# Optimization experiments

Measured on AMD Instinct MI355X. Metric: run time of the kernel, lower is better.

The kernel has to match this reference:

```python
import jax, jax.numpy as jnp
import numpy as np

D = 1024
H = 16
HD = D // H
MLP = 4 * D


def _lin(key, fin, fout):
    k1, k2 = jax.random.split(key)
    lim = 1.0 / np.sqrt(fin)
    W = jax.random.uniform(k1, (fin, fout), minval=-lim, maxval=lim, dtype=jnp.float32)
    b = jax.random.uniform(k2, (fout,), minval=-lim, maxval=lim, dtype=jnp.float32)
    return W, b


def setup_inputs() -> dict:
    key = jax.random.key(0)
    ks = jax.random.split(key, 10)
    x = jax.random.normal(ks[0], (4, 2048, D), dtype=jnp.float32)
    time_emb = jax.random.normal(ks[1], (4, D), dtype=jnp.float32)
    Wqkv, bqkv = _lin(ks[2], D, 3 * D)
    Wproj, bproj = _lin(ks[3], D, D)
    W1, b1 = _lin(ks[4], D, MLP)
    W2, b2 = _lin(ks[5], MLP, D)
    Wt, bt = _lin(ks[6], D, 6 * D)
    g1 = jnp.ones((D,), jnp.float32); be1 = jnp.zeros((D,), jnp.float32)
    g2 = jnp.ones((D,), jnp.float32); be2 = jnp.zeros((D,), jnp.float32)
    return {"x": x, "time_emb": time_emb, "Wqkv": Wqkv, "bqkv": bqkv,
            "Wproj": Wproj, "bproj": bproj, "W1": W1, "b1": b1, "W2": W2, "b2": b2,
            "Wt": Wt, "bt": bt, "g1": g1, "be1": be1, "g2": g2, "be2": be2}


def layernorm(x, g, b, eps=1e-5):
    mu = jnp.mean(x, axis=-1, keepdims=True)
    var = jnp.var(x, axis=-1, keepdims=True)
    return (x - mu) * jax.lax.rsqrt(var + eps) * g + b


def attention(h, Wqkv, bqkv, Wproj, bproj):
    B, L, _ = h.shape
    qkv = (h @ Wqkv + bqkv).reshape(B, L, 3, H, HD)
    q, k, v = jnp.moveaxis(qkv, 2, 0)  # each [B,L,H,HD]
    scale = HD ** -0.5
    attn = jnp.einsum('blhd,bmhd->bhlm', q, k) * scale
    attn = jax.nn.softmax(attn, axis=-1)
    out = jnp.einsum('bhlm,bmhd->blhd', attn, v).reshape(B, L, D)
    return out @ Wproj + bproj


def reference(x, time_emb, Wqkv, bqkv, Wproj, bproj, W1, b1, W2, b2, Wt, bt, g1, be1, g2, be2):
    tp = (jax.nn.silu(time_emb) @ Wt + bt)[:, None, :]  # [B,1,6D]
    shift_msa, scale_msa, gate_msa, shift_mlp, scale_mlp, gate_mlp = jnp.split(tp, 6, axis=-1)
    h = layernorm(x, g1, be1)
    h = h * (1.0 + scale_msa) + shift_msa
    h = attention(h, Wqkv, bqkv, Wproj, bproj)
    x = x + gate_msa * h
    h = layernorm(x, g2, be2)
    h = h * (1.0 + scale_mlp) + shift_mlp
    h = jax.nn.gelu(h @ W1 + b1, approximate=False) @ W2 + b2
    x = x + gate_mlp * h
    return x
```

## Files before the change

kernel.cpp:

```cpp
#include <hip/hip_runtime.h>
#include <hip/hip_bf16.h>
#include <math.h>


typedef __attribute__((ext_vector_type(8))) __bf16 bf16x8;
typedef __attribute__((ext_vector_type(4))) float f32x4;

union FragU { uint4 u; bf16x8 b; };

#define AS1(p) ((const __attribute__((address_space(1))) void*)(p))
#define AS3(p) ((__attribute__((address_space(3))) void*)(p))

__device__ __forceinline__ float bflo(uint u) {
    union { uint i; float f; } v; v.i = u << 16; return v.f;
}
__device__ __forceinline__ ushort f2bf(float f) {
    union { float f; uint i; } v; v.f = f;
    uint r = (v.i + 0x7fffu + ((v.i >> 16) & 1u)) >> 16;
    return (ushort)r;
}
__device__ __forceinline__ uint pkbf(float a, float b) {
    return __builtin_amdgcn_perm(__float_as_uint(b), __float_as_uint(a), 0x07060302u);
}
__device__ __forceinline__ void stval(ushort* p, float v) { *p = f2bf(v); }
__device__ __forceinline__ void stval(float* p, float v) { *p = v; }

__device__ __forceinline__ float gelu_f(float x) {
    float y = 0.7978845608f * (x + 0.044715f * x * x * x);
    float e = exp2f(y * 2.88539008178f);
    float t = 1.f - 2.f / (1.f + e);
    return 0.5f * x * (1.f + t);
}

__global__ __launch_bounds__(256) void transpose_f2b(const float* __restrict__ in,
                                                     ushort* __restrict__ out,
                                                     int R, int C) {
    __shared__ ushort t[32][33];
    int c0 = blockIdx.x * 32, r0 = blockIdx.y * 32;
    int tx = threadIdx.x, ty = threadIdx.y;
#pragma unroll
    for (int i = 0; i < 32; i += 8)
        t[ty + i][tx] = f2bf(in[(size_t)(r0 + ty + i) * C + c0 + tx]);
    __syncthreads();
#pragma unroll
    for (int i = 0; i < 32; i += 8)
        out[(size_t)(c0 + ty + i) * R + r0 + tx] = t[tx][ty + i];
}

__global__ __launch_bounds__(256) void transpose_v(const ushort* __restrict__ qkv,
                                                   ushort* __restrict__ vT) {
    int bh = blockIdx.x >> 5, lt = blockIdx.x & 31;
    int b = bh >> 4, h = bh & 15;
    int d = threadIdx.x & 63, lg = threadIdx.x >> 6;
    const ushort* src = qkv + (size_t)b * 2048 * 3072 + 2048 + h * 64 + d;
#pragma unroll
    for (int g = 0; g < 2; g++) {
        int l0 = lt * 64 + lg * 16 + g * 8;
        ushort v[8];
#pragma unroll
        for (int i = 0; i < 8; i++) v[i] = src[(size_t)(l0 + i) * 3072];
        *(uint4*)&vT[((size_t)bh * 64 + d) * 2048 + l0] = *(uint4*)v;
    }
}

__global__ __launch_bounds__(256) void tp_gemm(const float* __restrict__ te,
                                               const ushort* __restrict__ WtT,
                                               const float* __restrict__ bt,
                                               float* __restrict__ tp) {
    int w = blockIdx.x * 4 + (threadIdx.x >> 6);
    int lane = threadIdx.x & 63;
    int b = w / 6144, n = w % 6144;
    const ushort* wr = WtT + (size_t)n * 1024;
    const float* tr = te + (size_t)b * 1024;
    float s = 0.f;
#pragma unroll
    for (int i = 0; i < 16; i++) {
        int k = lane + 64 * i;
        float t = tr[k];
        float sil = t / (1.f + __expf(-t));
        s += sil * bflo((uint)wr[k]);
    }
#pragma unroll
    for (int x = 32; x; x >>= 1) s += __shfl_xor(s, x);
    if (lane == 0) tp[(size_t)b * 6144 + n] = s + bt[n];
}

__global__ __launch_bounds__(256) void ln_mod(const float* __restrict__ x,
                                              const float* __restrict__ tpb,
                                              const float* __restrict__ g,
                                              const float* __restrict__ be,
                                              ushort* __restrict__ out,
                                              int shift_off, int scale_off) {
    __shared__ float2 sred[4];
    int row = blockIdx.x;
    int b = row >> 11;
    int tid = threadIdx.x;
    float4 f = *(const float4*)&x[(size_t)row * 1024 + tid * 4];
    float v[4] = {f.x, f.y, f.z, f.w};
    float s = v[0] + v[1] + v[2] + v[3];
    float s2 = v[0] * v[0] + v[1] * v[1] + v[2] * v[2] + v[3] * v[3];
#pragma unroll
    for (int m = 32; m; m >>= 1) { s += __shfl_xor(s, m); s2 += __shfl_xor(s2, m); }
    if ((tid & 63) == 0) sred[tid >> 6] = make_float2(s, s2);
    __syncthreads();
    s = sred[0].x + sred[1].x + sred[2].x + sred[3].x;
    s2 = sred[0].y + sred[1].y + sred[2].y + sred[3].y;
    float mu = s * (1.f / 1024.f);
    float var = s2 * (1.f / 1024.f) - mu * mu;
    float rs = rsqrtf(var + 1e-5f);
    const float* tprow = tpb + (size_t)b * 6144;
    ushort o4[4];
#pragma unroll
    for (int t = 0; t < 4; t++) {
        int c = tid * 4 + t;
        float y = (v[t] - mu) * rs * g[c] + be[c];
        y = y * (1.f + tprow[scale_off + c]) + tprow[shift_off + c];
        o4[t] = f2bf(y);
    }
    *(uint2*)&out[(size_t)row * 1024 + tid * 4] = *(uint2*)o4;
}

template <int EPI, typename OT>
__global__ __launch_bounds__(256) void gemm_bt(const ushort* __restrict__ A,
                                               const ushort* __restrict__ BT,
                                               const float* __restrict__ bias,
                                               OT* __restrict__ C,
                                               int M, int N, int K,
                                               const float* __restrict__ res,
                                               const float* __restrict__ tpb,
                                               int goff, int sccols) {
    __shared__ __align__(16) ushort As[2][128 * 32];
    __shared__ __align__(16) ushort Bs[2][128 * 32];
    int m0 = blockIdx.y * 128, n0 = blockIdx.x * 128;
    int tid = threadIdx.x;
    int wid = tid >> 6, lane = tid & 63;
    int wy = wid >> 1, wx = wid & 1;
    int r16 = lane & 15;
    int q8 = (lane >> 4) << 3;

    f32x4 acc[4][4];
#pragma unroll
    for (int i = 0; i < 4; i++)
#pragma unroll
        for (int j = 0; j < 4; j++) acc[i][j] = (f32x4){0.f, 0.f, 0.f, 0.f};

    int sr = tid >> 2;
    int sc = (tid & 3) << 3;
    const ushort* Abase = A + (size_t)(m0 + sr) * K + sc;
    const ushort* Bbase = BT + (size_t)(n0 + sr) * K + sc;

    for (int k0 = 0; k0 < K; k0 += 64) {
#pragma unroll
        for (int c = 0; c < 2; c++) {
            ushort* AsW = As[c] + wid * 512;
            ushort* BsW = Bs[c] + wid * 512;
            int kk = k0 + 32 * c;
            __builtin_amdgcn_global_load_lds(AS1(Abase + kk), AS3(AsW), 16, 0, 0);
            __builtin_amdgcn_global_load_lds(AS1(Abase + (size_t)64 * K + kk), AS3(AsW + 2048), 16, 0, 0);
            __builtin_amdgcn_global_load_lds(AS1(Bbase + kk), AS3(BsW), 16, 0, 0);
            __builtin_amdgcn_global_load_lds(AS1(Bbase + (size_t)64 * K + kk), AS3(BsW + 2048), 16, 0, 0);
        }
        __syncthreads();
#pragma unroll
        for (int c = 0; c < 2; c++) {
            FragU fa[4], fb[4];
#pragma unroll
            for (int i = 0; i < 4; i++)
                fa[i].u = *(const uint4*)&As[c][(wy * 64 + i * 16 + r16) * 32 + q8];
#pragma unroll
            for (int j = 0; j < 4; j++)
                fb[j].u = *(const uint4*)&Bs[c][(wx * 64 + j * 16 + r16) * 32 + q8];
#pragma unroll
            for (int i = 0; i < 4; i++)
#pragma unroll
                for (int j = 0; j < 4; j++)
                    acc[i][j] = __builtin_amdgcn_mfma_f32_16x16x32_bf16(fa[i].b, fb[j].b, acc[i][j], 0, 0, 0);
        }
        __syncthreads();
    }

    int q4 = (lane >> 4) << 2;
#pragma unroll
    for (int i = 0; i < 4; i++) {
#pragma unroll
        for (int j = 0; j < 4; j++) {
            int col = n0 + wx * 64 + j * 16 + r16;
            float bv = bias[col];
#pragma unroll
            for (int t = 0; t < 4; t++) {
                int row = m0 + wy * 64 + i * 16 + q4 + t;
                float v = acc[i][j][t] + bv;
                if constexpr (EPI == 0) {
                    if (col < sccols) v *= 0.18033688011f;
                }
                if constexpr (EPI == 1) {
                    v = gelu_f(v);
                }
                if constexpr (EPI == 2) {
                    float rv = res[(size_t)row * N + col];
                    float gate = tpb[(size_t)(row >> 11) * 6144 + goff + col];
                    v = rv + gate * v;
                }
                stval(&C[(size_t)row * N + col], v);
            }
        }
    }
}

__global__ __launch_bounds__(512, 6) void attn_mfma(const ushort* __restrict__ qkv,
                                                    const ushort* __restrict__ vT,
                                                    ushort* __restrict__ out) {
    __shared__ __align__(16) ushort Ks[2][64 * 72];
    __shared__ __align__(16) ushort Vs[2][64 * 72];
    __shared__ __align__(16) ushort Ps[128 * 72];

    int tid = threadIdx.x;
    int wid = tid >> 6, lane = tid & 63;
    int r16 = lane & 15, quad = lane >> 4;
    int q8 = quad << 3, q4 = quad << 2;

    int bh = blockIdx.x >> 4;
    int qt = blockIdx.x & 15;
    int b = bh >> 4, h = bh & 15;
    const ushort* qkbase = qkv + (size_t)b * 2048 * 3072 + h * 64;

    int kr = tid >> 3;
    int kc = (tid & 7) << 3;
    const ushort* kptr = qkbase + 1024 + (size_t)kr * 3072 + kc;
    const ushort* vptr = vT + (size_t)bh * 131072 + (size_t)kr * 2048 + kc;

    uint4 ka = *(const uint4*)kptr;
    uint4 va = *(const uint4*)vptr;

    {
        int r = tid >> 2;
        int c = (tid & 3) << 4;
        const ushort* qp = qkbase + (size_t)(qt * 128 + r) * 3072 + c;
        *(uint4*)&Ps[r * 72 + c] = *(const uint4*)qp;
        *(uint4*)&Ps[r * 72 + c + 8] = *(const uint4*)(qp + 8);
    }
    __syncthreads();
    FragU qa[2];
#pragma unroll
    for (int ks = 0; ks < 2; ks++)
        qa[ks].u = *(const uint4*)&Ps[(wid * 16 + r16) * 72 + ks * 32 + q8];

    *(uint4*)&Ks[0][kr * 72 + kc] = ka;
    *(uint4*)&Vs[0][kr * 72 + kc] = va;
    ka = *(const uint4*)(kptr + (size_t)64 * 3072);
    va = *(const uint4*)(vptr + 64);
    __syncthreads();

    float l4[4] = {0.f, 0.f, 0.f, 0.f};
    f32x4 o[4];
#pragma unroll
    for (int dn = 0; dn < 4; dn++) o[dn] = (f32x4){0.f, 0.f, 0.f, 0.f};

    for (int kt = 0; kt < 32; kt++) {
        int cur = kt & 1;
        const ushort* ksb = Ks[cur];
        const ushort* vsb = Vs[cur];

        if (kt < 31) {
            *(uint4*)&Ks[cur ^ 1][kr * 72 + kc] = ka;
            *(uint4*)&Vs[cur ^ 1][kr * 72 + kc] = va;
        }
        if (kt < 30) {
            ka = *(const uint4*)(kptr + (size_t)(kt + 2) * 64 * 3072);
            va = *(const uint4*)(vptr + (kt + 2) * 64);
        }

        f32x4 s[4];
#pragma unroll
        for (int n = 0; n < 4; n++) s[n] = (f32x4){0.f, 0.f, 0.f, 0.f};
#pragma unroll
        for (int ks = 0; ks < 2; ks++) {
            FragU kb[4];
#pragma unroll
            for (int n = 0; n < 4; n++)
                kb[n].u = *(const uint4*)&ksb[(n * 16 + r16) * 72 + ks * 32 + q8];
#pragma unroll
            for (int n = 0; n < 4; n++)
                s[n] = __builtin_amdgcn_mfma_f32_16x16x32_bf16(kb[n].b, qa[ks].b, s[n], 0, 0, 0);
        }

        float p[4][4];
#pragma unroll
        for (int n = 0; n < 4; n++)
#pragma unroll
            for (int t = 0; t < 4; t++) {
                float pv = exp2f(s[n][t]);
                p[n][t] = pv;
                l4[t] += pv;
            }

#pragma unroll
        for (int n = 0; n < 4; n++) {
            uint2 w2 = make_uint2(pkbf(p[n][0], p[n][1]), pkbf(p[n][2], p[n][3]));
            *(uint2*)&Ps[(wid * 16 + r16) * 72 + n * 16 + q4] = w2;
        }

#pragma unroll
        for (int ks = 0; ks < 2; ks++) {
            FragU pa, vb[4];
            pa.u = *(const uint4*)&Ps[(wid * 16 + r16) * 72 + ks * 32 + q8];
#pragma unroll
            for (int dn = 0; dn < 4; dn++)
                vb[dn].u = *(const uint4*)&vsb[(dn * 16 + r16) * 72 + ks * 32 + q8];
#pragma unroll
            for (int dn = 0; dn < 4; dn++)
                o[dn] = __builtin_amdgcn_mfma_f32_16x16x32_bf16(vb[dn].b, pa.b, o[dn], 0, 0, 0);
        }

        __syncthreads();
    }

    float l_ = (l4[0] + l4[1]) + (l4[2] + l4[3]);
    l_ += __shfl_xor(l_, 16);
    l_ += __shfl_xor(l_, 32);
    float inv = 1.f / l_;
    int row = qt * 128 + wid * 16 + r16;
    ushort* orow = out + (size_t)(b * 2048 + row) * 1024 + h * 64;
#pragma unroll
    for (int dn = 0; dn < 4; dn++) {
        uint2 w2 = make_uint2(pkbf(o[dn][0] * inv, o[dn][1] * inv),
                              pkbf(o[dn][2] * inv, o[dn][3] * inv));
        *(uint2*)&orow[dn * 16 + q4] = w2;
    }
}

extern "C" void kernel_launch(void* const* d_in, const int* in_sizes, int n_in,
                              void* d_out, int out_size, void* d_ws, size_t ws_size,
                              hipStream_t stream) {
    const float* x    = (const float*)d_in[0];
    const float* te   = (const float*)d_in[1];
    const float* Wqkv = (const float*)d_in[2];
    const float* bqkv = (const float*)d_in[3];
    const float* Wproj= (const float*)d_in[4];
    const float* bproj= (const float*)d_in[5];
    const float* W1   = (const float*)d_in[6];
    const float* b1   = (const float*)d_in[7];
    const float* W2   = (const float*)d_in[8];
    const float* b2   = (const float*)d_in[9];
    const float* Wt   = (const float*)d_in[10];
    const float* bt   = (const float*)d_in[11];
    const float* g1   = (const float*)d_in[12];
    const float* be1  = (const float*)d_in[13];
    const float* g2   = (const float*)d_in[14];
    const float* be2  = (const float*)d_in[15];

    char* ws = (char*)d_ws;
    ushort* WqkvT  = (ushort*)(ws + 0);
    ushort* WprojT = (ushort*)(ws + 6291456);
    ushort* W1T    = (ushort*)(ws + 8388608);
    ushort* W2T    = (ushort*)(ws + 16777216);
    ushort* WtT    = (ushort*)(ws + 25165824);
    float*  tpb    = (float*)(ws + 37748736);
    ushort* hbuf   = (ushort*)(ws + 37847040);
    ushort* vTb    = (ushort*)(ws + 37847040);
    ushort* qkvb   = (ushort*)(ws + 54624256);
    ushort* midb   = (ushort*)(ws + 54624256);
    ushort* attnb  = (ushort*)(ws + 121733120);
    float*  x1b    = (float*)(ws + 138510336);

    dim3 tb(32, 8);
    hipLaunchKernelGGL(transpose_f2b, dim3(3072 / 32, 1024 / 32), tb, 0, stream, Wqkv, WqkvT, 1024, 3072);
    hipLaunchKernelGGL(transpose_f2b, dim3(1024 / 32, 1024 / 32), tb, 0, stream, Wproj, WprojT, 1024, 1024);
    hipLaunchKernelGGL(transpose_f2b, dim3(4096 / 32, 1024 / 32), tb, 0, stream, W1, W1T, 1024, 4096);
    hipLaunchKernelGGL(transpose_f2b, dim3(1024 / 32, 4096 / 32), tb, 0, stream, W2, W2T, 4096, 1024);
    hipLaunchKernelGGL(transpose_f2b, dim3(6144 / 32, 1024 / 32), tb, 0, stream, Wt, WtT, 1024, 6144);

    hipLaunchKernelGGL(tp_gemm, dim3(6144), dim3(256), 0, stream, te, WtT, bt, tpb);

    hipLaunchKernelGGL(ln_mod, dim3(8192), dim3(256), 0, stream, x, tpb, g1, be1, hbuf, 0, 1024);

    hipLaunchKernelGGL((gemm_bt<0, ushort>), dim3(3072 / 128, 8192 / 128), dim3(256), 0, stream,
                       hbuf, WqkvT, bqkv, qkvb, 8192, 3072, 1024, (const float*)nullptr, (const float*)nullptr, 0, 1024);

    hipLaunchKernelGGL(transpose_v, dim3(2048), dim3(256), 0, stream, qkvb, vTb);

    hipLaunchKernelGGL(attn_mfma, dim3(1024), dim3(512), 0, stream, qkvb, vTb, attnb);

    hipLaunchKernelGGL((gemm_bt<2, float>), dim3(1024 / 128, 8192 / 128), dim3(256), 0, stream,
                       attnb, WprojT, bproj, x1b, 8192, 1024, 1024, x, tpb, 2048, 0);

    hipLaunchKernelGGL(ln_mod, dim3(8192), dim3(256), 0, stream, x1b, tpb, g2, be2, hbuf, 3072, 4096);

    hipLaunchKernelGGL((gemm_bt<1, ushort>), dim3(4096 / 128, 8192 / 128), dim3(256), 0, stream,
                       hbuf, W1T, b1, midb, 8192, 4096, 1024, (const float*)nullptr, (const float*)nullptr, 0, 0);

    hipLaunchKernelGGL((gemm_bt<2, float>), dim3(1024 / 128, 8192 / 128), dim3(256), 0, stream,
                       midb, W2T, b2, (float*)d_out, 8192, 1024, 4096, x1b, tpb, 5120, 0);
}
```

Measured before the change: 639.1 us.

## Double per-wave query rows in attention to reuse K/V tiles across 256-row blocks

The attention kernel now gives each block 256 query rows instead of 128, so each wave handles two 16-row query sub-tiles. Each K and V fragment loaded from shared memory is reused for both sub-tiles, and the grid is halved. This cuts K/V global and LDS traffic per query row. In exchange it raises register and LDS use (launch bounds lowered to 4 blocks), which may reduce occupancy, and with only 512 blocks the GPU may be less evenly filled.

```diff
diff --git a/kernel.cpp b/kernel.cpp
--- a/kernel.cpp
+++ b/kernel.cpp
@@ -207,20 +207,20 @@
     }
 }
 
-__global__ __launch_bounds__(512, 6) void attn_mfma(const ushort* __restrict__ qkv,
+__global__ __launch_bounds__(512, 4) void attn_mfma(const ushort* __restrict__ qkv,
                                                     const ushort* __restrict__ vT,
                                                     ushort* __restrict__ out) {
     __shared__ __align__(16) ushort Ks[2][64 * 72];
     __shared__ __align__(16) ushort Vs[2][64 * 72];
-    __shared__ __align__(16) ushort Ps[128 * 72];
+    __shared__ __align__(16) ushort Ps[256 * 72];
 
     int tid = threadIdx.x;
     int wid = tid >> 6, lane = tid & 63;
     int r16 = lane & 15, quad = lane >> 4;
     int q8 = quad << 3, q4 = quad << 2;
 
-    int bh = blockIdx.x >> 4;
-    int qt = blockIdx.x & 15;
+    int bh = blockIdx.x >> 3;
+    int qt = blockIdx.x & 7;
     int b = bh >> 4, h = bh & 15;
     const ushort* qkbase = qkv + (size_t)b * 2048 * 3072 + h * 64;
 
@@ -233,17 +233,21 @@
     uint4 va = *(const uint4*)vptr;
 
     {
-        int r = tid >> 2;
-        int c = (tid & 3) << 4;
-        const ushort* qp = qkbase + (size_t)(qt * 128 + r) * 3072 + c;
-        *(uint4*)&Ps[r * 72 + c] = *(const uint4*)qp;
-        *(uint4*)&Ps[r * 72 + c + 8] = *(const uint4*)(qp + 8);
+        int r = tid >> 1;
+        int c = (tid & 1) << 5;
+        const ushort* qp = qkbase + (size_t)(qt * 256 + r) * 3072 + c;
+        *(uint4*)&Ps[r * 72 + c]      = *(const uint4*)qp;
+        *(uint4*)&Ps[r * 72 + c + 8]  = *(const uint4*)(qp + 8);
+        *(uint4*)&Ps[r * 72 + c + 16] = *(const uint4*)(qp + 16);
+        *(uint4*)&Ps[r * 72 + c + 24] = *(const uint4*)(qp + 24);
     }
     __syncthreads();
-    FragU qa[2];
-#pragma unroll
-    for (int ks = 0; ks < 2; ks++)
-        qa[ks].u = *(const uint4*)&Ps[(wid * 16 + r16) * 72 + ks * 32 + q8];
+    FragU qa[2][2];
+#pragma unroll
+    for (int qm = 0; qm < 2; qm++)
+#pragma unroll
+        for (int ks = 0; ks < 2; ks++)
+            qa[qm][ks].u = *(const uint4*)&Ps[(wid * 32 + qm * 16 + r16) * 72 + ks * 32 + q8];
 
     *(uint4*)&Ks[0][kr * 72 + kc] = ka;
     *(uint4*)&Vs[0][kr * 72 + kc] = va;
@@ -251,10 +255,12 @@
     va = *(const uint4*)(vptr + 64);
     __syncthreads();
 
-    float l4[4] = {0.f, 0.f, 0.f, 0.f};
-    f32x4 o[4];
-#pragma unroll
-    for (int dn = 0; dn < 4; dn++) o[dn] = (f32x4){0.f, 0.f, 0.f, 0.f};
+    float l4[2][4] = {{0.f, 0.f, 0.f, 0.f}, {0.f, 0.f, 0.f, 0.f}};
+    f32x4 o[2][4];
+#pragma unroll
+    for (int qm = 0; qm < 2; qm++)
+#pragma unroll
+        for (int dn = 0; dn < 4; dn++) o[qm][dn] = (f32x4){0.f, 0.f, 0.f, 0.f};
 
     for (int kt = 0; kt < 32; kt++) {
         int cur = kt & 1;
@@ -265,67 +271,72 @@
             *(uint4*)&Ks[cur ^ 1][kr * 72 + kc] = ka;
             *(uint4*)&Vs[cur ^ 1][kr * 72 + kc] = va;
         }
+
+        FragU kb[2][4];
+#pragma unroll
+        for (int ks = 0; ks < 2; ks++)
+#pragma unroll
+            for (int n = 0; n < 4; n++)
+                kb[ks][n].u = *(const uint4*)&ksb[(n * 16 + r16) * 72 + ks * 32 + q8];
+#pragma unroll
+        for (int qm = 0; qm < 2; qm++) {
+            f32x4 s[4];
+#pragma unroll
+            for (int n = 0; n < 4; n++) s[n] = (f32x4){0.f, 0.f, 0.f, 0.f};
+#pragma unroll
+            for (int ks = 0; ks < 2; ks++)
+#pragma unroll
+                for (int n = 0; n < 4; n++)
+                    s[n] = __builtin_amdgcn_mfma_f32_16x16x32_bf16(kb[ks][n].b, qa[qm][ks].b, s[n], 0, 0, 0);
+#pragma unroll
+            for (int n = 0; n < 4; n++) {
+                float p0 = exp2f(s[n][0]);
+                float p1 = exp2f(s[n][1]);
+                float p2 = exp2f(s[n][2]);
+                float p3 = exp2f(s[n][3]);
+                l4[qm][0] += p0; l4[qm][1] += p1; l4[qm][2] += p2; l4[qm][3] += p3;
+                uint2 w2 = make_uint2(pkbf(p0, p1), pkbf(p2, p3));
+                *(uint2*)&Ps[(wid * 32 + qm * 16 + r16) * 72 + n * 16 + q4] = w2;
+            }
+        }
+
         if (kt < 30) {
             ka = *(const uint4*)(kptr + (size_t)(kt + 2) * 64 * 3072);
             va = *(const uint4*)(vptr + (kt + 2) * 64);
         }
 
-        f32x4 s[4];
-#pragma unroll
-        for (int n = 0; n < 4; n++) s[n] = (f32x4){0.f, 0.f, 0.f, 0.f};
 #pragma unroll
         for (int ks = 0; ks < 2; ks++) {
-            FragU kb[4];
-#pragma unroll
-            for (int n = 0; n < 4; n++)
-                kb[n].u = *(const uint4*)&ksb[(n * 16 + r16) * 72 + ks * 32 + q8];
-#pragma unroll
-            for (int n = 0; n < 4; n++)
-                s[n] = __builtin_amdgcn_mfma_f32_16x16x32_bf16(kb[n].b, qa[ks].b, s[n], 0, 0, 0);
-        }
-
-        float p[4][4];
-#pragma unroll
-        for (int n = 0; n < 4; n++)
-#pragma unroll
-            for (int t = 0; t < 4; t++) {
-                float pv = exp2f(s[n][t]);
-                p[n][t] = pv;
-                l4[t] += pv;
-            }
-
-#pragma unroll
-        for (int n = 0; n < 4; n++) {
-            uint2 w2 = make_uint2(pkbf(p[n][0], p[n][1]), pkbf(p[n][2], p[n][3]));
-            *(uint2*)&Ps[(wid * 16 + r16) * 72 + n * 16 + q4] = w2;
-        }
-
-#pragma unroll
-        for (int ks = 0; ks < 2; ks++) {
-            FragU pa, vb[4];
-            pa.u = *(const uint4*)&Ps[(wid * 16 + r16) * 72 + ks * 32 + q8];
+            FragU vb[4], pa0, pa1;
 #pragma unroll
             for (int dn = 0; dn < 4; dn++)
                 vb[dn].u = *(const uint4*)&vsb[(dn * 16 + r16) * 72 + ks * 32 + q8];
-#pragma unroll
-            for (int dn = 0; dn < 4; dn++)
-                o[dn] = __builtin_amdgcn_mfma_f32_16x16x32_bf16(vb[dn].b, pa.b, o[dn], 0, 0, 0);
+            pa0.u = *(const uint4*)&Ps[(wid * 32 + r16) * 72 + ks * 32 + q8];
+            pa1.u = *(const uint4*)&Ps[(wid * 32 + 16 + r16) * 72 + ks * 32 + q8];
+#pragma unroll
+            for (int dn = 0; dn < 4; dn++) {
+                o[0][dn] = __builtin_amdgcn_mfma_f32_16x16x32_bf16(vb[dn].b, pa0.b, o[0][dn], 0, 0, 0);
+                o[1][dn] = __builtin_amdgcn_mfma_f32_16x16x32_bf16(vb[dn].b, pa1.b, o[1][dn], 0, 0, 0);
+            }
         }
 
         __syncthreads();
     }
 
-    float l_ = (l4[0] + l4[1]) + (l4[2] + l4[3]);
-    l_ += __shfl_xor(l_, 16);
-    l_ += __shfl_xor(l_, 32);
-    float inv = 1.f / l_;
-    int row = qt * 128 + wid * 16 + r16;
-    ushort* orow = out + (size_t)(b * 2048 + row) * 1024 + h * 64;
-#pragma unroll
-    for (int dn = 0; dn < 4; dn++) {
-        uint2 w2 = make_uint2(pkbf(o[dn][0] * inv, o[dn][1] * inv),
-                              pkbf(o[dn][2] * inv, o[dn][3] * inv));
-        *(uint2*)&orow[dn * 16 + q4] = w2;
+#pragma unroll
+    for (int qm = 0; qm < 2; qm++) {
+        float l_ = (l4[qm][0] + l4[qm][1]) + (l4[qm][2] + l4[qm][3]);
+        l_ += __shfl_xor(l_, 16);
+        l_ += __shfl_xor(l_, 32);
+        float inv = 1.f / l_;
+        int row = qt * 256 + wid * 32 + qm * 16 + r16;
+        ushort* orow = out + (size_t)(b * 2048 + row) * 1024 + h * 64;
+#pragma unroll
+        for (int dn = 0; dn < 4; dn++) {
+            uint2 w2 = make_uint2(pkbf(o[qm][dn][0] * inv, o[qm][dn][1] * inv),
+                                  pkbf(o[qm][dn][2] * inv, o[qm][dn][3] * inv));
+            *(uint2*)&orow[dn * 16 + q4] = w2;
+        }
     }
 }
 
@@ -379,7 +390,7 @@
 
     hipLaunchKernelGGL(transpose_v, dim3(2048), dim3(256), 0, stream, qkvb, vTb);
 
-    hipLaunchKernelGGL(attn_mfma, dim3(1024), dim3(512), 0, stream, qkvb, vTb, attnb);
+    hipLaunchKernelGGL(attn_mfma, dim3(512), dim3(512), 0, stream, qkvb, vTb, attnb);
 
     hipLaunchKernelGGL((gemm_bt<2, float>), dim3(1024 / 128, 8192 / 128), dim3(256), 0, stream,
                        attnb, WprojT, bproj, x1b, 8192, 1024, 1024, x, tpb, 2048, 0);
```

Result: faster. 622.2 us (-2.7%).
